# Optimization experiments

Hardware: AMD Instinct MI355X
Metric: run time of the kernel (lower is better)

## Reference

```python
import jax, jax.numpy as jnp
import numpy as np

H = 8  # number_heads

def setup_inputs() -> dict:
    key = jax.random.key(0)
    ks = jax.random.split(key, 10)
    B, Nx, Ny, Qd, Kd, Vd = 4, 2048, 2048, 512, 512, 512
    s = 0.02
    return {
        "X": jax.random.normal(ks[0], (B, Nx, Qd), jnp.float32),
        "Y": jax.random.normal(ks[1], (B, Ny, Kd), jnp.float32),
        "Wq": jax.random.normal(ks[2], (Vd, Qd), jnp.float32) * s,
        "bq": jax.random.normal(ks[3], (Vd,), jnp.float32) * s,
        "Wk": jax.random.normal(ks[4], (Vd, Kd), jnp.float32) * s,
        "bk": jax.random.normal(ks[5], (Vd,), jnp.float32) * s,
        "Wv": jax.random.normal(ks[6], (Vd, Kd), jnp.float32) * s,
        "bv": jax.random.normal(ks[7], (Vd,), jnp.float32) * s,
        "Wo": jax.random.normal(ks[8], (Vd, Vd), jnp.float32) * s,
        "bo": jax.random.normal(ks[9], (Vd,), jnp.float32) * s,
    }

def reference(X, Y, Wq, bq, Wk, bk, Wv, bv, Wo, bo):
    B, Nq, _ = X.shape
    Nk = Y.shape[1]
    Vd = Wq.shape[0]
    d = Vd // H  # head dim (dim_split)
    # QKV projections (torch Linear: x @ W^T + b)
    Q = (X @ Wq.T + bq).reshape(B, Nq, H, d)
    K = (Y @ Wk.T + bk).reshape(B, Nk, H, d)
    V = (Y @ Wv.T + bv).reshape(B, Nk, H, d)
    # attention: softmax(Q K^T / sqrt(d)) per head
    scores = jnp.einsum("bqhd,bkhd->bhqk", Q, K) / jnp.sqrt(jnp.float32(d))
    attn = jax.nn.softmax(scores, axis=-1)
    # residual on Q (pre-output-proj), per the original: O = Q_split + Attn @ V_split
    O = Q + jnp.einsum("bhqk,bkhd->bqhd", attn, V)
    O = O.reshape(B, Nq, Vd)  # concat heads back
    return O @ Wo.T + bo
```

## Files before the change

kernel.cpp:

```cpp
#include <hip/hip_runtime.h>
#include <hip/hip_bf16.h>

typedef unsigned short u16;
typedef __attribute__((ext_vector_type(4))) float f32x4;
typedef __attribute__((ext_vector_type(16))) float f32x16;
typedef __attribute__((ext_vector_type(8))) short bf16x8;
typedef __attribute__((ext_vector_type(4))) int i32x4;
typedef __attribute__((ext_vector_type(4))) unsigned short u16x4;

#define DEVI static __device__ __forceinline__

DEVI u16 f2bf(float f) {
  __hip_bfloat16 h = __float2bfloat16(f);
  return *reinterpret_cast<u16*>(&h);
}
DEVI float bf2f(u16 u) {
  unsigned int x = ((unsigned int)u) << 16;
  return __uint_as_float(x);
}
DEVI float exp2a(float x) {
  float r;
  asm("v_exp_f32 %0, %1" : "=v"(r) : "v"(x));
  return r;
}
DEVI int cvtpk(float lo, float hi) {
  int r;
  asm("v_cvt_pk_bf16_f32 %0, %1, %2" : "=v"(r) : "v"(lo), "v"(hi));
  return r;
}
DEVI f32x16 mfma32(bf16x8 a, bf16x8 b, f32x16 c) {
  return __builtin_amdgcn_mfma_f32_32x32x16_bf16(a, b, c, 0, 0, 0);
}
DEVI float xhalf_sum(float x) {
  float a = x, b;
  asm volatile("v_mov_b32 %0, %1" : "=v"(b) : "v"(x));
  asm volatile("v_permlane32_swap_b32 %0, %1" : "+v"(a), "+v"(b));
  return a + b;
}

DEVI void gload_lds16(const void* g, void* l) {
  __builtin_amdgcn_global_load_lds(
      (const __attribute__((address_space(1))) unsigned int*)g,
      (__attribute__((address_space(3))) unsigned int*)l, 16, 0, 0);
}

#define BAR() __builtin_amdgcn_s_barrier()
#define WAITV0() asm volatile("s_waitcnt vmcnt(0)" ::: "memory")
#define WAITV4() asm volatile("s_waitcnt vmcnt(4)" ::: "memory")

__global__ __launch_bounds__(256) void k_convall(
    const float* __restrict__ X, const float* __restrict__ Y,
    const float* __restrict__ Wq, const float* __restrict__ Wk,
    const float* __restrict__ Wv, const float* __restrict__ Wo,
    u16* __restrict__ Xb, u16* __restrict__ Yb, u16* __restrict__ Wb) {
  long i = ((long)blockIdx.x * 256 + threadIdx.x) * 8;
  const float* s;
  u16* d;
  long off;
  if (i < 4194304) {
    s = X; d = Xb; off = i;
  } else if (i < 8388608) {
    s = Y; d = Yb; off = i - 4194304;
  } else {
    long w = (i - 8388608) >> 18;
    off = (i - 8388608) & 262143;
    s = w == 0 ? Wq : w == 1 ? Wk : w == 2 ? Wv : Wo;
    d = Wb + w * 262144;
  }
  f32x4 a = *(const f32x4*)(s + off);
  f32x4 b = *(const f32x4*)(s + off + 4);
  bf16x8 v;
#pragma unroll
  for (int j = 0; j < 4; ++j) {
    v[j]     = (short)f2bf(a[j]);
    v[4 + j] = (short)f2bf(b[j]);
  }
  *(bf16x8*)(d + off) = v;
}

struct GemmAcc { f32x4 acc[4][2]; };

DEVI void gemm_body(const u16* __restrict__ A, const u16* __restrict__ Bw,
                    int m0, int n0, u16* As, u16* Bs, GemmAcc& G) {
  constexpr int K = 512;
  const int tid = threadIdx.x;
  const int wid = tid >> 6, lane = tid & 63;
  const int g = lane >> 4, li = lane & 15;
  const int wr = wid >> 1, wc = wid & 1;

#pragma unroll
  for (int mr = 0; mr < 4; ++mr)
#pragma unroll
    for (int nr = 0; nr < 2; ++nr) G.acc[mr][nr] = (f32x4){0.f, 0.f, 0.f, 0.f};

  for (int kt = 0; kt < K / 64; ++kt) {
    const int k0 = kt * 64;
#pragma unroll
    for (int i = 0; i < 4; ++i) {
      int P0 = ((i * 4 + wid) << 10) + lane * 16;
      int L0 = P0 ^ (((P0 >> 7) & 7) << 4);
      int row = L0 >> 7, colb = L0 & 127;
      gload_lds16((const char*)A + ((size_t)(m0 + row) * K + k0) * 2 + colb,
                  (char*)As + ((i * 4 + wid) << 10));
    }
#pragma unroll
    for (int i = 0; i < 2; ++i) {
      int P0 = ((i * 4 + wid) << 10) + lane * 16;
      int L0 = P0 ^ (((P0 >> 7) & 7) << 4);
      int row = L0 >> 7, colb = L0 & 127;
      gload_lds16((const char*)Bw + ((size_t)(n0 + row) * K + k0) * 2 + colb,
                  (char*)Bs + ((i * 4 + wid) << 10));
    }
    asm volatile("s_waitcnt vmcnt(0)" ::: "memory");
    __syncthreads();

#pragma unroll
    for (int ks = 0; ks < 2; ++ks) {
      bf16x8 af[4], bfr[2];
#pragma unroll
      for (int mr = 0; mr < 4; ++mr) {
        int row = wr * 64 + mr * 16 + li;
        int L = row * 128 + ks * 64 + g * 16;
        int P = L ^ ((row & 7) << 4);
        af[mr] = *(const bf16x8*)((const char*)As + P);
      }
#pragma unroll
      for (int nr = 0; nr < 2; ++nr) {
        int row = wc * 32 + nr * 16 + li;
        int L = row * 128 + ks * 64 + g * 16;
        int P = L ^ ((row & 7) << 4);
        bfr[nr] = *(const bf16x8*)((const char*)Bs + P);
      }
#pragma unroll
      for (int mr = 0; mr < 4; ++mr)
#pragma unroll
        for (int nr = 0; nr < 2; ++nr)
          G.acc[mr][nr] = __builtin_amdgcn_mfma_f32_16x16x32_bf16(
              af[mr], bfr[nr], G.acc[mr][nr], 0, 0, 0);
    }
    __syncthreads();
  }
}

__global__ __launch_bounds__(256) void k_gemm_qkv(
    const u16* __restrict__ Xb, const u16* __restrict__ Yb,
    const u16* __restrict__ Wall, const float* __restrict__ bq,
    const float* __restrict__ bk, const float* __restrict__ bv,
    u16* __restrict__ Qb, u16* __restrict__ Kb, u16* __restrict__ Vtb) {
  __shared__ __align__(16) u16 As[128 * 64];
  __shared__ __align__(16) u16 Bs[64 * 64];
  const int z = blockIdx.z;
  const u16* A = z == 0 ? Xb : Yb;
  const u16* Bw = Wall + (size_t)z * 262144;
  const float* bias = z == 0 ? bq : (z == 1 ? bk : bv);
  u16* Cout = z == 0 ? Qb : (z == 1 ? Kb : Vtb);

  int lin = blockIdx.x + 8 * blockIdx.y;
  int xcd = lin & 7, slot = lin >> 3;
  int by = xcd * 8 + (slot >> 3), bx = slot & 7;
  const int m0 = by * 128, n0 = bx * 64;

  GemmAcc G;
  gemm_body(A, Bw, m0, n0, As, Bs, G);

  const int tid = threadIdx.x;
  const int wid = tid >> 6, lane = tid & 63;
  const int g = lane >> 4, li = lane & 15;
  const int wr = wid >> 1, wc = wid & 1;
#pragma unroll
  for (int nr = 0; nr < 2; ++nr) {
    int col = n0 + wc * 32 + nr * 16 + li;
    float bvv = bias[col];
#pragma unroll
    for (int mr = 0; mr < 4; ++mr) {
#pragma unroll
      for (int j = 0; j < 4; ++j) {
        int row = m0 + wr * 64 + mr * 16 + g * 4 + j;
        float v = G.acc[mr][nr][j] + bvv;
        int b = row >> 11, nn = row & 2047, h = col >> 6, dd = col & 63;
        if (z <= 1)
          Cout[(((size_t)(b * 8 + h) << 11) + nn) * 64 + dd] = f2bf(v);
        else
          Cout[(((size_t)(b * 8 + h) * 64) + dd) * 2048 + nn] = f2bf(v);
      }
    }
  }
}

__global__ __launch_bounds__(256) void k_gemm_out(const u16* __restrict__ A,
                                                  const u16* __restrict__ Bw,
                                                  const float* __restrict__ bias,
                                                  float* __restrict__ Cout) {
  __shared__ __align__(16) u16 As[128 * 64];
  __shared__ __align__(16) u16 Bs[64 * 64];
  int lin = blockIdx.x + 8 * blockIdx.y;
  int xcd = lin & 7, slot = lin >> 3;
  int by = xcd * 8 + (slot >> 3), bx = slot & 7;
  const int m0 = by * 128, n0 = bx * 64;

  GemmAcc G;
  gemm_body(A, Bw, m0, n0, As, Bs, G);

  const int tid = threadIdx.x;
  const int wid = tid >> 6, lane = tid & 63;
  const int g = lane >> 4, li = lane & 15;
  const int wr = wid >> 1, wc = wid & 1;
#pragma unroll
  for (int nr = 0; nr < 2; ++nr) {
    int col = n0 + wc * 32 + nr * 16 + li;
    float bvv = bias[col];
#pragma unroll
    for (int mr = 0; mr < 4; ++mr) {
#pragma unroll
      for (int j = 0; j < 4; ++j) {
        int row = m0 + wr * 64 + mr * 16 + g * 4 + j;
        Cout[(size_t)row * 512 + col] = G.acc[mr][nr][j] + bvv;
      }
    }
  }
}

DEVI void qk_tile(const char* L, int KB, const int* vK, const bf16x8* qf,
                  f32x16& r0, f32x16& r1) {
  const f32x16 Z = {};
  bf16x8 kf;
  __builtin_amdgcn_s_setprio(1);
  kf = *(const bf16x8*)(L + (vK[0] + KB));        r0 = mfma32(kf, qf[0], Z);
  kf = *(const bf16x8*)(L + (vK[1] + KB));        r0 = mfma32(kf, qf[1], r0);
  kf = *(const bf16x8*)(L + (vK[2] + KB));        r0 = mfma32(kf, qf[2], r0);
  kf = *(const bf16x8*)(L + (vK[3] + KB));        r0 = mfma32(kf, qf[3], r0);
  kf = *(const bf16x8*)(L + (vK[0] + KB + 4096)); r1 = mfma32(kf, qf[0], Z);
  kf = *(const bf16x8*)(L + (vK[1] + KB + 4096)); r1 = mfma32(kf, qf[1], r1);
  kf = *(const bf16x8*)(L + (vK[2] + KB + 4096)); r1 = mfma32(kf, qf[2], r1);
  kf = *(const bf16x8*)(L + (vK[3] + KB + 4096)); r1 = mfma32(kf, qf[3], r1);
  __builtin_amdgcn_s_setprio(0);
}

DEVI void softmax_pv(const char* L, int VB, const int* vK, f32x16& s0, f32x16& s1,
                     f32x16& o0, f32x16& o1, float& lsum) {
#pragma unroll
  for (int i = 0; i < 16; ++i) s0[i] = exp2a(s0[i]);
#pragma unroll
  for (int i = 0; i < 16; ++i) s1[i] = exp2a(s1[i]);
  float t8[8];
#pragma unroll
  for (int i = 0; i < 8; ++i)
    t8[i] = (s0[2 * i] + s0[2 * i + 1]) + (s1[2 * i] + s1[2 * i + 1]);
  lsum += ((t8[0] + t8[1]) + (t8[2] + t8[3])) + ((t8[4] + t8[5]) + (t8[6] + t8[7]));

  __builtin_amdgcn_s_setprio(1);
#pragma unroll
  for (int kt16 = 0; kt16 < 4; ++kt16) {
    const f32x16& sp = (kt16 & 2) ? s1 : s0;
    const int base = (kt16 & 1) * 8;
    int a0 = cvtpk(sp[base + 0], sp[base + 1]);
    int a1 = cvtpk(sp[base + 2], sp[base + 3]);
    int b0 = cvtpk(sp[base + 4], sp[base + 5]);
    int b1 = cvtpk(sp[base + 6], sp[base + 7]);
    asm volatile("v_permlane32_swap_b32 %0, %1" : "+v"(a0), "+v"(b0));
    asm volatile("v_permlane32_swap_b32 %0, %1" : "+v"(a1), "+v"(b1));
    i32x4 pi = {a0, a1, b0, b1};
    bf16x8 pb = __builtin_bit_cast(bf16x8, pi);
    bf16x8 va = *(const bf16x8*)(L + (vK[kt16] + VB));
    o0 = mfma32(va, pb, o0);
    va = *(const bf16x8*)(L + (vK[kt16] + VB + 4096));
    o1 = mfma32(va, pb, o1);
  }
  __builtin_amdgcn_s_setprio(0);
}

__global__ __launch_bounds__(512, 4) void k_attn(const u16* __restrict__ Qb,
                                                 const u16* __restrict__ Kb,
                                                 const u16* __restrict__ Vt,
                                                 u16* __restrict__ Ob) {
  __shared__ __align__(16) u16 lds[32768];
  const int tid = threadIdx.x, wid = tid >> 6, lane = tid & 63;
  const int li = lane & 31, h = lane >> 5;
  const int grp = wid >> 2, w4 = wid & 3;

  const int lin = blockIdx.x;
  const int xcd = lin & 7, slot = lin >> 3;
  const int bh = xcd * 4 + (slot >> 4);
  const int qt = slot & 15;
  const int start = (slot * 2) & 15;

  const u16* Qh = Qb + ((size_t)bh << 11) * 64;
  const u16* Kh = Kb + ((size_t)bh << 11) * 64;
  const u16* Vh = Vt + (size_t)bh * 64 * 2048;

  const int swz = (li & 7) << 4;
  int vK[4];
#pragma unroll
  for (int k4 = 0; k4 < 4; ++k4) vK[k4] = li * 128 + ((k4 * 32 + h * 16) ^ swz);

  const int q = qt * 128 + w4 * 32 + li;
  const float C2 = 0.18033688f;
  bf16x8 qf[4];
#pragma unroll
  for (int k4 = 0; k4 < 4; ++k4) {
    bf16x8 f = *(const bf16x8*)(Qh + (size_t)q * 64 + k4 * 16 + h * 8);
    bf16x8 r;
#pragma unroll
    for (int e = 0; e < 4; ++e) {
      float a = bf2f((u16)f[2 * e]) * C2;
      float b = bf2f((u16)f[2 * e + 1]) * C2;
      int p = cvtpk(a, b);
      r[2 * e]     = (short)(p & 0xffff);
      r[2 * e + 1] = (short)((unsigned)p >> 16);
    }
    qf[k4] = r;
  }

  int P0a = (w4 << 10) + lane * 16;
  int L0a = P0a ^ (((P0a >> 7) & 7) << 4);
  int P0b = ((4 + w4) << 10) + lane * 16;
  int L0b = P0b ^ (((P0b >> 7) & 7) << 4);
  const int vA = (L0a >> 7) * 4096 + (L0a & 127);
  const int vB = (L0b >> 7) * 4096 + (L0b & 127);
  char* lb = (char*)lds + grp * 32768;
  const char* L = (const char*)lb;

  auto T = [&](int n) { return grp * 16 + ((start + n) & 15); };
  auto stageK = [&](int tt, int kb) {
    const char* src = (const char*)Kh + (size_t)tt * 8192;
    gload_lds16(src + L0a, lb + kb + (w4 << 10));
    gload_lds16(src + L0b, lb + kb + ((4 + w4) << 10));
  };
  auto stageV = [&](int tt, int vb) {
    const char* src = (const char*)Vh + (size_t)tt * 128;
    gload_lds16(src + vA, lb + vb + (w4 << 10));
    gload_lds16(src + vB, lb + vb + ((4 + w4) << 10));
  };

  f32x16 o0 = {}, o1 = {};
  f32x16 s0, s1;
  float lsum = 0.f;

  stageK(T(0), 0);
  stageV(T(0), 16384);
  stageK(T(1), 8192);
  stageV(T(1), 24576);
  WAITV4();
  BAR();

#pragma unroll 1
  for (int it = 0; it < 14; ++it) {
    const int cur = (it & 1) * 8192;
    qk_tile(L, cur, vK, qf, s0, s1);
    softmax_pv(L, 16384 + cur, vK, s0, s1, o0, o1, lsum);
    BAR();
    stageK(T(it + 2), cur);
    stageV(T(it + 2), 16384 + cur);
    WAITV4();
    BAR();
  }
  qk_tile(L, 0, vK, qf, s0, s1);
  softmax_pv(L, 16384, vK, s0, s1, o0, o1, lsum);
  WAITV0();
  BAR();
  qk_tile(L, 8192, vK, qf, s0, s1);
  softmax_pv(L, 24576, vK, s0, s1, o0, o1, lsum);

  __syncthreads();
  if (grp == 1) {
#pragma unroll
    for (int j = 0; j < 8; ++j) {
      const f32x16& o = (j < 4) ? o0 : o1;
      const int s2 = (j & 3) * 4;
      f32x4 c = {o[s2 + 0], o[s2 + 1], o[s2 + 2], o[s2 + 3]};
      *(f32x4*)((char*)lds + w4 * 8192 + j * 1024 + lane * 16) = c;
    }
    ((float*)((char*)lds + 32768))[w4 * 64 + lane] = lsum;
  }
  __syncthreads();
  if (grp == 0) {
#pragma unroll
    for (int j = 0; j < 8; ++j) {
      f32x4 c = *(const f32x4*)((const char*)lds + w4 * 8192 + j * 1024 + lane * 16);
      f32x16& o = (j < 4) ? o0 : o1;
      const int s2 = (j & 3) * 4;
      o[s2 + 0] += c[0]; o[s2 + 1] += c[1]; o[s2 + 2] += c[2]; o[s2 + 3] += c[3];
    }
    lsum += ((const float*)((const char*)lds + 32768))[w4 * 64 + lane];
    const float inv = 1.0f / xhalf_sum(lsum);

    const int b = bh >> 3, head = bh & 7;
    u16* orow = Ob + ((size_t)(b * 2048 + q)) * 512 + head * 64;
    const u16* qrow = Qh + (size_t)q * 64;
#pragma unroll
    for (int dt = 0; dt < 2; ++dt) {
      const f32x16& o = dt ? o1 : o0;
#pragma unroll
      for (int s2 = 0; s2 < 4; ++s2) {
        int d0 = dt * 32 + s2 * 8 + h * 4;
        u16x4 qv = *(const u16x4*)(qrow + d0);
        u16x4 w;
#pragma unroll
        for (int j = 0; j < 4; ++j)
          w[j] = f2bf(fmaf(o[s2 * 4 + j], inv, bf2f(qv[j])));
        *(u16x4*)(orow + d0) = w;
      }
    }
  }
}

extern "C" void kernel_launch(void* const* d_in, const int* in_sizes, int n_in,
                              void* d_out, int out_size, void* d_ws, size_t ws_size,
                              hipStream_t stream) {
  const float* X  = (const float*)d_in[0];
  const float* Y  = (const float*)d_in[1];
  const float* Wq = (const float*)d_in[2];
  const float* bq = (const float*)d_in[3];
  const float* Wk = (const float*)d_in[4];
  const float* bk = (const float*)d_in[5];
  const float* Wv = (const float*)d_in[6];
  const float* bv = (const float*)d_in[7];
  const float* Wo = (const float*)d_in[8];
  const float* bo = (const float*)d_in[9];

  char* ws = (char*)d_ws;
  u16* Xb  = (u16*)(ws);
  u16* Yb  = (u16*)(ws + (size_t)(8  << 20));
  u16* Wb  = (u16*)(ws + (size_t)(16 << 20));
  u16* Qb  = (u16*)(ws + (size_t)(18 << 20));
  u16* Kb  = (u16*)(ws + (size_t)(26 << 20));
  u16* Vtb = (u16*)(ws + (size_t)(34 << 20));
  u16* Ob  = (u16*)(ws + (size_t)(42 << 20));

  k_convall<<<4608, 256, 0, stream>>>(X, Y, Wq, Wk, Wv, Wo, Xb, Yb, Wb);

  k_gemm_qkv<<<dim3(8, 64, 3), 256, 0, stream>>>(Xb, Yb, Wb, bq, bk, bv, Qb, Kb, Vtb);

  k_attn<<<512, 512, 0, stream>>>(Qb, Kb, Vtb, Ob);

  k_gemm_out<<<dim3(8, 64), 256, 0, stream>>>(Ob, Wb + 3 * 262144, bo, (float*)d_out);
}
```

Baseline: 96.49 us.

## Double-buffer GEMM loads, swap V-proj operands, and software-pipeline attention with smaller tiles

The GEMM body now double-buffers its A/B tiles in shared memory, so the next k-tile's global loads overlap the current MFMA work instead of waiting on a full drain. The V projection swaps operands so its transposed output is written along contiguous rows, avoiding strided stores. The attention kernel moves to 32-key tiles with a split pipeline: the QK product for the next tile is issued before softmax and PV for the current one, and K/V staging is interleaved between the two. The setprio hints are dropped and LDS use is halved, at the cost of more barriers and more complex staging.

```diff
diff --git a/kernel.cpp b/kernel.cpp
--- a/kernel.cpp
+++ b/kernel.cpp
@@ -46,7 +46,7 @@
 
 #define BAR() __builtin_amdgcn_s_barrier()
 #define WAITV0() asm volatile("s_waitcnt vmcnt(0)" ::: "memory")
-#define WAITV4() asm volatile("s_waitcnt vmcnt(4)" ::: "memory")
+#define WAITV1() asm volatile("s_waitcnt vmcnt(1)" ::: "memory")
 
 __global__ __launch_bounds__(256) void k_convall(
     const float* __restrict__ X, const float* __restrict__ Y,
@@ -81,39 +81,53 @@
 struct GemmAcc { f32x4 acc[4][2]; };
 
 DEVI void gemm_body(const u16* __restrict__ A, const u16* __restrict__ Bw,
-                    int m0, int n0, u16* As, u16* Bs, GemmAcc& G) {
-  constexpr int K = 512;
+                    int m0, int n0, char* sm, GemmAcc& G) {
   const int tid = threadIdx.x;
   const int wid = tid >> 6, lane = tid & 63;
   const int g = lane >> 4, li = lane & 15;
   const int wr = wid >> 1, wc = wid & 1;
 
+  int arow[4], acol[4];
+#pragma unroll
+  for (int i = 0; i < 4; ++i) {
+    int P0 = ((i * 4 + wid) << 10) + lane * 16;
+    int L0 = P0 ^ (((P0 >> 7) & 7) << 4);
+    arow[i] = L0 >> 7;
+    acol[i] = L0 & 127;
+  }
+
 #pragma unroll
   for (int mr = 0; mr < 4; ++mr)
 #pragma unroll
     for (int nr = 0; nr < 2; ++nr) G.acc[mr][nr] = (f32x4){0.f, 0.f, 0.f, 0.f};
 
-  for (int kt = 0; kt < K / 64; ++kt) {
-    const int k0 = kt * 64;
-#pragma unroll
-    for (int i = 0; i < 4; ++i) {
-      int P0 = ((i * 4 + wid) << 10) + lane * 16;
-      int L0 = P0 ^ (((P0 >> 7) & 7) << 4);
-      int row = L0 >> 7, colb = L0 & 127;
-      gload_lds16((const char*)A + ((size_t)(m0 + row) * K + k0) * 2 + colb,
-                  (char*)As + ((i * 4 + wid) << 10));
-    }
-#pragma unroll
-    for (int i = 0; i < 2; ++i) {
-      int P0 = ((i * 4 + wid) << 10) + lane * 16;
-      int L0 = P0 ^ (((P0 >> 7) & 7) << 4);
-      int row = L0 >> 7, colb = L0 & 127;
-      gload_lds16((const char*)Bw + ((size_t)(n0 + row) * K + k0) * 2 + colb,
-                  (char*)Bs + ((i * 4 + wid) << 10));
-    }
-    asm volatile("s_waitcnt vmcnt(0)" ::: "memory");
-    __syncthreads();
-
+  auto stage = [&](int kt, int half) {
+    char* As = sm + half * 24576;
+    char* Bs = As + 16384;
+    const int k0b = kt * 128;
+#pragma unroll
+    for (int i = 0; i < 4; ++i)
+      gload_lds16((const char*)A + (size_t)(m0 + arow[i]) * 1024 + k0b + acol[i],
+                  As + ((i * 4 + wid) << 10));
+#pragma unroll
+    for (int i = 0; i < 2; ++i)
+      gload_lds16((const char*)Bw + (size_t)(n0 + arow[i]) * 1024 + k0b + acol[i],
+                  Bs + ((i * 4 + wid) << 10));
+  };
+
+  stage(0, 0);
+#pragma unroll 1
+  for (int kt = 0; kt < 8; ++kt) {
+    const int half = kt & 1;
+    if (kt < 7) {
+      stage(kt + 1, half ^ 1);
+      asm volatile("s_waitcnt vmcnt(6)" ::: "memory");
+    } else {
+      asm volatile("s_waitcnt vmcnt(0)" ::: "memory");
+    }
+    BAR();
+    const char* As = sm + half * 24576;
+    const char* Bs = As + 16384;
 #pragma unroll
     for (int ks = 0; ks < 2; ++ks) {
       bf16x8 af[4], bfr[2];
@@ -122,14 +136,14 @@
         int row = wr * 64 + mr * 16 + li;
         int L = row * 128 + ks * 64 + g * 16;
         int P = L ^ ((row & 7) << 4);
-        af[mr] = *(const bf16x8*)((const char*)As + P);
+        af[mr] = *(const bf16x8*)(As + P);
       }
 #pragma unroll
       for (int nr = 0; nr < 2; ++nr) {
         int row = wc * 32 + nr * 16 + li;
         int L = row * 128 + ks * 64 + g * 16;
         int P = L ^ ((row & 7) << 4);
-        bfr[nr] = *(const bf16x8*)((const char*)Bs + P);
+        bfr[nr] = *(const bf16x8*)(Bs + P);
       }
 #pragma unroll
       for (int mr = 0; mr < 4; ++mr)
@@ -138,7 +152,7 @@
           G.acc[mr][nr] = __builtin_amdgcn_mfma_f32_16x16x32_bf16(
               af[mr], bfr[nr], G.acc[mr][nr], 0, 0, 0);
     }
-    __syncthreads();
+    BAR();
   }
 }
 
@@ -147,21 +161,83 @@
     const u16* __restrict__ Wall, const float* __restrict__ bq,
     const float* __restrict__ bk, const float* __restrict__ bv,
     u16* __restrict__ Qb, u16* __restrict__ Kb, u16* __restrict__ Vtb) {
-  __shared__ __align__(16) u16 As[128 * 64];
-  __shared__ __align__(16) u16 Bs[64 * 64];
+  __shared__ __align__(16) char sm[49152];
   const int z = blockIdx.z;
-  const u16* A = z == 0 ? Xb : Yb;
-  const u16* Bw = Wall + (size_t)z * 262144;
-  const float* bias = z == 0 ? bq : (z == 1 ? bk : bv);
-  u16* Cout = z == 0 ? Qb : (z == 1 ? Kb : Vtb);
-
+  int lin = blockIdx.x + 8 * blockIdx.y;
+  int xcd = lin & 7, slot = lin >> 3;
+
+  const u16 *Ag, *Bg;
+  int m0, n0;
+  if (z == 2) {
+    Ag = Wall + 2 * 262144;
+    Bg = Yb;
+    m0 = (slot >> 4) * 128;
+    n0 = (xcd * 16 + (slot & 15)) * 64;
+  } else {
+    Ag = z ? Yb : Xb;
+    Bg = Wall + (size_t)z * 262144;
+    m0 = (xcd * 8 + (slot >> 3)) * 128;
+    n0 = (slot & 7) * 64;
+  }
+
+  GemmAcc G;
+  gemm_body(Ag, Bg, m0, n0, sm, G);
+
+  const int tid = threadIdx.x;
+  const int wid = tid >> 6, lane = tid & 63;
+  const int g = lane >> 4, li = lane & 15;
+  const int wr = wid >> 1, wc = wid & 1;
+
+  if (z <= 1) {
+    u16* Cout = z ? Kb : Qb;
+    const float* bias = z ? bk : bq;
+#pragma unroll
+    for (int nr = 0; nr < 2; ++nr) {
+      int col = n0 + wc * 32 + nr * 16 + li;
+      float bvv = bias[col];
+#pragma unroll
+      for (int mr = 0; mr < 4; ++mr) {
+#pragma unroll
+        for (int j = 0; j < 4; ++j) {
+          int row = m0 + wr * 64 + mr * 16 + g * 4 + j;
+          float v = G.acc[mr][nr][j] + bvv;
+          int b = row >> 11, nn = row & 2047, h = col >> 6, dd = col & 63;
+          Cout[(((size_t)(b * 8 + h) << 11) + nn) * 64 + dd] = f2bf(v);
+        }
+      }
+    }
+  } else {
+#pragma unroll
+    for (int mr = 0; mr < 4; ++mr) {
+#pragma unroll
+      for (int j = 0; j < 4; ++j) {
+        int row = m0 + wr * 64 + mr * 16 + g * 4 + j;
+        float bvv = bv[row];
+        int hh = row >> 6, dd = row & 63;
+#pragma unroll
+        for (int nr = 0; nr < 2; ++nr) {
+          int col = n0 + wc * 32 + nr * 16 + li;
+          int b = col >> 11, nn = col & 2047;
+          Vtb[(((size_t)(b * 8 + hh) * 64) + dd) * 2048 + nn] =
+              f2bf(G.acc[mr][nr][j] + bvv);
+        }
+      }
+    }
+  }
+}
+
+__global__ __launch_bounds__(256) void k_gemm_out(const u16* __restrict__ A,
+                                                  const u16* __restrict__ Bw,
+                                                  const float* __restrict__ bias,
+                                                  float* __restrict__ Cout) {
+  __shared__ __align__(16) char sm[49152];
   int lin = blockIdx.x + 8 * blockIdx.y;
   int xcd = lin & 7, slot = lin >> 3;
   int by = xcd * 8 + (slot >> 3), bx = slot & 7;
   const int m0 = by * 128, n0 = bx * 64;
 
   GemmAcc G;
-  gemm_body(A, Bw, m0, n0, As, Bs, G);
+  gemm_body(A, Bw, m0, n0, sm, G);
 
   const int tid = threadIdx.x;
   const int wid = tid >> 6, lane = tid & 63;
@@ -176,104 +252,54 @@
 #pragma unroll
       for (int j = 0; j < 4; ++j) {
         int row = m0 + wr * 64 + mr * 16 + g * 4 + j;
-        float v = G.acc[mr][nr][j] + bvv;
-        int b = row >> 11, nn = row & 2047, h = col >> 6, dd = col & 63;
-        if (z <= 1)
-          Cout[(((size_t)(b * 8 + h) << 11) + nn) * 64 + dd] = f2bf(v);
-        else
-          Cout[(((size_t)(b * 8 + h) * 64) + dd) * 2048 + nn] = f2bf(v);
-      }
-    }
-  }
-}
-
-__global__ __launch_bounds__(256) void k_gemm_out(const u16* __restrict__ A,
-                                                  const u16* __restrict__ Bw,
-                                                  const float* __restrict__ bias,
-                                                  float* __restrict__ Cout) {
-  __shared__ __align__(16) u16 As[128 * 64];
-  __shared__ __align__(16) u16 Bs[64 * 64];
-  int lin = blockIdx.x + 8 * blockIdx.y;
-  int xcd = lin & 7, slot = lin >> 3;
-  int by = xcd * 8 + (slot >> 3), bx = slot & 7;
-  const int m0 = by * 128, n0 = bx * 64;
-
-  GemmAcc G;
-  gemm_body(A, Bw, m0, n0, As, Bs, G);
-
-  const int tid = threadIdx.x;
-  const int wid = tid >> 6, lane = tid & 63;
-  const int g = lane >> 4, li = lane & 15;
-  const int wr = wid >> 1, wc = wid & 1;
-#pragma unroll
-  for (int nr = 0; nr < 2; ++nr) {
-    int col = n0 + wc * 32 + nr * 16 + li;
-    float bvv = bias[col];
-#pragma unroll
-    for (int mr = 0; mr < 4; ++mr) {
-#pragma unroll
-      for (int j = 0; j < 4; ++j) {
-        int row = m0 + wr * 64 + mr * 16 + g * 4 + j;
         Cout[(size_t)row * 512 + col] = G.acc[mr][nr][j] + bvv;
       }
     }
   }
 }
 
-DEVI void qk_tile(const char* L, int KB, const int* vK, const bf16x8* qf,
-                  f32x16& r0, f32x16& r1) {
+DEVI void qk32(const char* L, int KB, const int* vK, const bf16x8* qf, f32x16& r) {
   const f32x16 Z = {};
   bf16x8 kf;
-  __builtin_amdgcn_s_setprio(1);
-  kf = *(const bf16x8*)(L + (vK[0] + KB));        r0 = mfma32(kf, qf[0], Z);
-  kf = *(const bf16x8*)(L + (vK[1] + KB));        r0 = mfma32(kf, qf[1], r0);
-  kf = *(const bf16x8*)(L + (vK[2] + KB));        r0 = mfma32(kf, qf[2], r0);
-  kf = *(const bf16x8*)(L + (vK[3] + KB));        r0 = mfma32(kf, qf[3], r0);
-  kf = *(const bf16x8*)(L + (vK[0] + KB + 4096)); r1 = mfma32(kf, qf[0], Z);
-  kf = *(const bf16x8*)(L + (vK[1] + KB + 4096)); r1 = mfma32(kf, qf[1], r1);
-  kf = *(const bf16x8*)(L + (vK[2] + KB + 4096)); r1 = mfma32(kf, qf[2], r1);
-  kf = *(const bf16x8*)(L + (vK[3] + KB + 4096)); r1 = mfma32(kf, qf[3], r1);
-  __builtin_amdgcn_s_setprio(0);
-}
-
-DEVI void softmax_pv(const char* L, int VB, const int* vK, f32x16& s0, f32x16& s1,
-                     f32x16& o0, f32x16& o1, float& lsum) {
-#pragma unroll
-  for (int i = 0; i < 16; ++i) s0[i] = exp2a(s0[i]);
-#pragma unroll
-  for (int i = 0; i < 16; ++i) s1[i] = exp2a(s1[i]);
-  float t8[8];
-#pragma unroll
-  for (int i = 0; i < 8; ++i)
-    t8[i] = (s0[2 * i] + s0[2 * i + 1]) + (s1[2 * i] + s1[2 * i + 1]);
-  lsum += ((t8[0] + t8[1]) + (t8[2] + t8[3])) + ((t8[4] + t8[5]) + (t8[6] + t8[7]));
-
-  __builtin_amdgcn_s_setprio(1);
-#pragma unroll
-  for (int kt16 = 0; kt16 < 4; ++kt16) {
-    const f32x16& sp = (kt16 & 2) ? s1 : s0;
-    const int base = (kt16 & 1) * 8;
-    int a0 = cvtpk(sp[base + 0], sp[base + 1]);
-    int a1 = cvtpk(sp[base + 2], sp[base + 3]);
-    int b0 = cvtpk(sp[base + 4], sp[base + 5]);
-    int b1 = cvtpk(sp[base + 6], sp[base + 7]);
+  kf = *(const bf16x8*)(L + (vK[0] + KB)); r = mfma32(kf, qf[0], Z);
+  kf = *(const bf16x8*)(L + (vK[1] + KB)); r = mfma32(kf, qf[1], r);
+  kf = *(const bf16x8*)(L + (vK[2] + KB)); r = mfma32(kf, qf[2], r);
+  kf = *(const bf16x8*)(L + (vK[3] + KB)); r = mfma32(kf, qf[3], r);
+}
+
+DEVI void sm_pv32(const char* L, int VB, const int* vV, f32x16& s,
+                  f32x16& o0, f32x16& o1, float& lsum) {
+#pragma unroll
+  for (int i = 0; i < 16; ++i) s[i] = exp2a(s[i]);
+  float t4[4];
+#pragma unroll
+  for (int i = 0; i < 4; ++i)
+    t4[i] = (s[4 * i] + s[4 * i + 1]) + (s[4 * i + 2] + s[4 * i + 3]);
+  lsum += (t4[0] + t4[1]) + (t4[2] + t4[3]);
+
+#pragma unroll
+  for (int kt = 0; kt < 2; ++kt) {
+    const int base = kt * 8;
+    int a0 = cvtpk(s[base + 0], s[base + 1]);
+    int a1 = cvtpk(s[base + 2], s[base + 3]);
+    int b0 = cvtpk(s[base + 4], s[base + 5]);
+    int b1 = cvtpk(s[base + 6], s[base + 7]);
     asm volatile("v_permlane32_swap_b32 %0, %1" : "+v"(a0), "+v"(b0));
     asm volatile("v_permlane32_swap_b32 %0, %1" : "+v"(a1), "+v"(b1));
     i32x4 pi = {a0, a1, b0, b1};
     bf16x8 pb = __builtin_bit_cast(bf16x8, pi);
-    bf16x8 va = *(const bf16x8*)(L + (vK[kt16] + VB));
+    bf16x8 va = *(const bf16x8*)(L + (vV[kt] + VB));
     o0 = mfma32(va, pb, o0);
-    va = *(const bf16x8*)(L + (vK[kt16] + VB + 4096));
+    va = *(const bf16x8*)(L + (vV[kt] + VB + 2048));
     o1 = mfma32(va, pb, o1);
   }
-  __builtin_amdgcn_s_setprio(0);
 }
 
 __global__ __launch_bounds__(512, 4) void k_attn(const u16* __restrict__ Qb,
                                                  const u16* __restrict__ Kb,
                                                  const u16* __restrict__ Vt,
                                                  u16* __restrict__ Ob) {
-  __shared__ __align__(16) u16 lds[32768];
+  __shared__ __align__(16) char lds[33792];
   const int tid = threadIdx.x, wid = tid >> 6, lane = tid & 63;
   const int li = lane & 31, h = lane >> 5;
   const int grp = wid >> 2, w4 = wid & 3;
@@ -282,16 +308,21 @@
   const int xcd = lin & 7, slot = lin >> 3;
   const int bh = xcd * 4 + (slot >> 4);
   const int qt = slot & 15;
-  const int start = (slot * 2) & 15;
+  const int start = (slot * 3) & 31;
 
   const u16* Qh = Qb + ((size_t)bh << 11) * 64;
   const u16* Kh = Kb + ((size_t)bh << 11) * 64;
   const u16* Vh = Vt + (size_t)bh * 64 * 2048;
 
-  const int swz = (li & 7) << 4;
-  int vK[4];
-#pragma unroll
-  for (int k4 = 0; k4 < 4; ++k4) vK[k4] = li * 128 + ((k4 * 32 + h * 16) ^ swz);
+  int vK[4], vV[2];
+  {
+    const int swzK = (li & 7) << 4;
+#pragma unroll
+    for (int k4 = 0; k4 < 4; ++k4) vK[k4] = li * 128 + ((k4 * 32 + h * 16) ^ swzK);
+    const int swzV = (li & 3) << 4;
+#pragma unroll
+    for (int kt = 0; kt < 2; ++kt) vV[kt] = li * 64 + ((kt * 32 + h * 16) ^ swzV);
+  }
 
   const int q = qt * 128 + w4 * 32 + li;
   const float C2 = 0.18033688f;
@@ -302,64 +333,66 @@
     bf16x8 r;
 #pragma unroll
     for (int e = 0; e < 4; ++e) {
-      float a = bf2f((u16)f[2 * e]) * C2;
-      float b = bf2f((u16)f[2 * e + 1]) * C2;
-      int p = cvtpk(a, b);
+      int p = cvtpk(bf2f((u16)f[2 * e]) * C2, bf2f((u16)f[2 * e + 1]) * C2);
       r[2 * e]     = (short)(p & 0xffff);
       r[2 * e + 1] = (short)((unsigned)p >> 16);
     }
     qf[k4] = r;
   }
 
-  int P0a = (w4 << 10) + lane * 16;
-  int L0a = P0a ^ (((P0a >> 7) & 7) << 4);
-  int P0b = ((4 + w4) << 10) + lane * 16;
-  int L0b = P0b ^ (((P0b >> 7) & 7) << 4);
-  const int vA = (L0a >> 7) * 4096 + (L0a & 127);
-  const int vB = (L0b >> 7) * 4096 + (L0b & 127);
-  char* lb = (char*)lds + grp * 32768;
-  const char* L = (const char*)lb;
-
-  auto T = [&](int n) { return grp * 16 + ((start + n) & 15); };
+  const int PK = (w4 << 10) + (lane << 4);
+  const int LK = PK ^ (((PK >> 7) & 7) << 4);
+  const int LV = PK ^ (((PK >> 6) & 3) << 4);
+  const int vgo = (LV >> 6) * 4096 + (LV & 63);
+
+  char* gb = lds + grp * 16384;
+  const char* Lg = gb;
+
+  auto T = [&](int n) { return grp * 32 + ((start + n) & 31); };
   auto stageK = [&](int tt, int kb) {
-    const char* src = (const char*)Kh + (size_t)tt * 8192;
-    gload_lds16(src + L0a, lb + kb + (w4 << 10));
-    gload_lds16(src + L0b, lb + kb + ((4 + w4) << 10));
+    gload_lds16((const char*)Kh + (size_t)tt * 4096 + LK, gb + kb + (w4 << 10));
   };
   auto stageV = [&](int tt, int vb) {
-    const char* src = (const char*)Vh + (size_t)tt * 128;
-    gload_lds16(src + vA, lb + vb + (w4 << 10));
-    gload_lds16(src + vB, lb + vb + ((4 + w4) << 10));
+    gload_lds16((const char*)Vh + (size_t)tt * 64 + vgo, gb + vb + (w4 << 10));
   };
 
   f32x16 o0 = {}, o1 = {};
-  f32x16 s0, s1;
+  f32x16 sA, sB;
   float lsum = 0.f;
 
   stageK(T(0), 0);
-  stageV(T(0), 16384);
-  stageK(T(1), 8192);
-  stageV(T(1), 24576);
-  WAITV4();
-  BAR();
-
-#pragma unroll 1
-  for (int it = 0; it < 14; ++it) {
-    const int cur = (it & 1) * 8192;
-    qk_tile(L, cur, vK, qf, s0, s1);
-    softmax_pv(L, 16384 + cur, vK, s0, s1, o0, o1, lsum);
-    BAR();
-    stageK(T(it + 2), cur);
-    stageV(T(it + 2), 16384 + cur);
-    WAITV4();
-    BAR();
-  }
-  qk_tile(L, 0, vK, qf, s0, s1);
-  softmax_pv(L, 16384, vK, s0, s1, o0, o1, lsum);
+  stageV(T(0), 8192);
+  stageK(T(1), 4096);
+  stageV(T(1), 12288);
   WAITV0();
   BAR();
-  qk_tile(L, 8192, vK, qf, s0, s1);
-  softmax_pv(L, 24576, vK, s0, s1, o0, o1, lsum);
+  qk32(Lg, 0, vK, qf, sA);
+
+#pragma unroll 1
+  for (int it = 0; it < 15; ++it) {
+    const int t = it * 2;
+    WAITV1();
+    BAR();
+    stageK(T(t + 2), 0);
+    qk32(Lg, 4096, vK, qf, sB);
+    sm_pv32(Lg, 8192, vV, sA, o0, o1, lsum);
+    BAR();
+    stageV(T(t + 2), 8192);
+    WAITV1();
+    BAR();
+    stageK(T(t + 3), 4096);
+    qk32(Lg, 0, vK, qf, sA);
+    sm_pv32(Lg, 12288, vV, sB, o0, o1, lsum);
+    BAR();
+    stageV(T(t + 3), 12288);
+  }
+  WAITV1();
+  BAR();
+  qk32(Lg, 4096, vK, qf, sB);
+  sm_pv32(Lg, 8192, vV, sA, o0, o1, lsum);
+  WAITV0();
+  BAR();
+  sm_pv32(Lg, 12288, vV, sB, o0, o1, lsum);
 
   __syncthreads();
   if (grp == 1) {
@@ -368,20 +401,20 @@
       const f32x16& o = (j < 4) ? o0 : o1;
       const int s2 = (j & 3) * 4;
       f32x4 c = {o[s2 + 0], o[s2 + 1], o[s2 + 2], o[s2 + 3]};
-      *(f32x4*)((char*)lds + w4 * 8192 + j * 1024 + lane * 16) = c;
-    }
-    ((float*)((char*)lds + 32768))[w4 * 64 + lane] = lsum;
+      *(f32x4*)(lds + w4 * 8192 + j * 1024 + lane * 16) = c;
+    }
+    ((float*)(lds + 32768))[w4 * 64 + lane] = lsum;
   }
   __syncthreads();
   if (grp == 0) {
 #pragma unroll
     for (int j = 0; j < 8; ++j) {
-      f32x4 c = *(const f32x4*)((const char*)lds + w4 * 8192 + j * 1024 + lane * 16);
+      f32x4 c = *(const f32x4*)(lds + w4 * 8192 + j * 1024 + lane * 16);
       f32x16& o = (j < 4) ? o0 : o1;
       const int s2 = (j & 3) * 4;
       o[s2 + 0] += c[0]; o[s2 + 1] += c[1]; o[s2 + 2] += c[2]; o[s2 + 3] += c[3];
     }
-    lsum += ((const float*)((const char*)lds + 32768))[w4 * 64 + lane];
+    lsum += ((const float*)(lds + 32768))[w4 * 64 + lane];
     const float inv = 1.0f / xhalf_sum(lsum);
 
     const int b = bh >> 3, head = bh & 7;
```

Result: faster. 88.30 us (-8.5%).
